# Performance work log

Hardware: AMD Instinct MI355X
Metric: run time of the kernel (lower is better)

Reference implementation:

```python
import jax, jax.numpy as jnp
import numpy as np

N_NODES = 20000
N_EDGES = 640000
C_IN = 128      # num_node_features
K_FOLDS = 8     # num_edge_features
FILTERS = 128


def setup_inputs() -> dict:
    key = jax.random.key(0)
    k1, k2, k3, k4, k5, k6 = jax.random.split(key, 6)
    node_features = jax.random.normal(k1, (N_NODES, C_IN), dtype=jnp.float32)
    edge_features = jax.random.uniform(k2, (K_FOLDS, N_EDGES), dtype=jnp.float32)
    rows = jax.random.randint(k3, (N_EDGES,), 0, N_NODES)
    cols = jax.random.randint(k4, (N_EDGES,), 0, N_NODES)
    indices = jnp.stack([rows, cols], axis=1).astype(jnp.int64)
    # glorot_uniform kernel [K, C_in, filters]
    limit = np.sqrt(6.0 / (C_IN + FILTERS))
    kernel = jax.random.uniform(k5, (K_FOLDS, C_IN, FILTERS), dtype=jnp.float32,
                                minval=-limit, maxval=limit)
    bias = jnp.zeros((FILTERS,), dtype=jnp.float32)
    return {
        "node_features": node_features,
        "edge_features": edge_features,
        "kernel": kernel,
        "bias": bias,
        "indices": indices,
        "out_size": N_NODES,
    }


def reference(node_features, edge_features, kernel, bias, indices, out_size):
    # fold_conv: out[i,f] = sum_{e: row(e)=i} sum_k ef[k,e] * (x[col(e)] @ kernel[k])[f]
    row = indices[:, 0]
    col = indices[:, 1]
    xg = node_features[col]  # [E, C] gathered source-node features
    E = xg.shape[0]
    msgs = jnp.zeros((E, kernel.shape[2]), dtype=node_features.dtype)
    # Loop over the small fixed number of folds (K=8); each iteration is a
    # dense [E,C]x[C,F] matmul scaled by the per-edge fold weight.
    for k in range(kernel.shape[0]):
        msgs = msgs + (xg @ kernel[k]) * edge_features[k][:, None]
    out = jax.ops.segment_sum(msgs, row, num_segments=out_size)  # [out_size, F]
    out = out + bias  # bias_add; activation is None (linear)
    return out
```

## Files before the change

kernel.cpp:

```cpp
#include <hip/hip_runtime.h>
#include <cstddef>
#include <cstdint>

static constexpr int kNodes   = 20000;
static constexpr int kEdges   = 640000;
static constexpr int kCin     = 128;
static constexpr int kFolds   = 8;
static constexpr int kFilters = 128;
static constexpr int kKdim    = kFolds * kCin;
static constexpr int kCap     = 80;

static constexpr int kNBucket = 250;
static constexpr int kRowsPB  = 80;
static constexpr int kCapB    = 3072;
static constexpr int kBin1Blk = 160;

typedef __attribute__((ext_vector_type(8))) short v8s;
typedef __attribute__((ext_vector_type(4))) float v4f;

__device__ __forceinline__ unsigned short f2bf(float f) {
    union { float f; uint32_t u; } v; v.f = f;
    const uint32_t u = v.u;
    return (unsigned short)((u + 0x7fffu + ((u >> 16) & 1u)) >> 16);
}
__device__ __forceinline__ float bf2f(unsigned short s) {
    union { uint32_t u; float f; } v; v.u = ((uint32_t)s) << 16;
    return v.f;
}

__global__ __launch_bounds__(256) void prep_k(
    const int2*  __restrict__ idx2,
    const float* __restrict__ ef,
    const float* __restrict__ x,
    const float* __restrict__ W,
    int* __restrict__ bucketCnt,
    int2* __restrict__ pairs,
    unsigned int* __restrict__ rec,
    unsigned short* __restrict__ xb,
    unsigned short* __restrict__ Wp)
{
    const int b = blockIdx.x;
    const int t = threadIdx.x;
    if (b < 2500) {
        const int e = b * 256 + t;
        const int2 rc = idx2[e];
        union { uint4 q; unsigned int w[4]; unsigned short s[8]; } o;
        #pragma unroll
        for (int k = 0; k < kFolds; ++k)
            o.s[k] = f2bf(ef[(size_t)k * kEdges + e]);
        uint4* recp = (uint4*)(rec + (size_t)e * 8);
        recp[0] = make_uint4((unsigned)rc.y, o.w[0], o.w[1], o.w[2]);
        recp[1] = make_uint4(o.w[3], 0u, 0u, 0u);
    } else if (b < 3750) {
        const int i = (b - 2500) * 2048 + t * 8;
        const float4 a = *(const float4*)(x + i);
        const float4 c = *(const float4*)(x + i + 4);
        union { uint4 q; unsigned short s[8]; } o;
        o.s[0] = f2bf(a.x); o.s[1] = f2bf(a.y); o.s[2] = f2bf(a.z); o.s[3] = f2bf(a.w);
        o.s[4] = f2bf(c.x); o.s[5] = f2bf(c.y); o.s[6] = f2bf(c.z); o.s[7] = f2bf(c.w);
        *(uint4*)(xb + i) = o.q;
    } else if (b < 3814) {
        const int t2 = (b - 3750) * 256 + t;
        const int n  = t2 & 127;
        const int k8 = t2 >> 7;
        const int c  = k8 >> 2;
        const int q  = k8 & 3;
        union { uint4 qv; unsigned short s[8]; } o;
        #pragma unroll
        for (int j = 0; j < 8; ++j)
            o.s[j] = f2bf(W[(size_t)(k8 * 8 + j) * kFilters + n]);
        *(uint4*)(Wp + (((size_t)c * kFilters + n) * 4 + q) * 8) = o.qv;
    } else {
        __shared__ int hist[kNBucket];
        __shared__ int base[kNBucket];
        const int bb = b - 3814;
        const int e0 = bb * 4096;

        if (t < kNBucket) hist[t] = 0;
        __syncthreads();

        int rowsReg[16];
        #pragma unroll
        for (int i = 0; i < 16; ++i) {
            const int e = e0 + i * 256 + t;
            int row = -1;
            if (e < kEdges) {
                row = idx2[e].x;
                atomicAdd(&hist[row / kRowsPB], 1);
            }
            rowsReg[i] = row;
        }
        __syncthreads();

        if (t < kNBucket) {
            const int h = hist[t];
            base[t] = atomicAdd(&bucketCnt[t], h);
            hist[t] = 0;
        }
        __syncthreads();

        #pragma unroll
        for (int i = 0; i < 16; ++i) {
            const int row = rowsReg[i];
            if (row >= 0) {
                const int e  = e0 + i * 256 + t;
                const int bk = row / kRowsPB;
                const int sl = base[bk] + atomicAdd(&hist[bk], 1);
                if (sl < kCapB)
                    pairs[(size_t)bk * kCapB + sl] = make_int2(row, e);
            }
        }
    }
}

__global__ __launch_bounds__(256) void bin2_k(
    const int2* __restrict__ pairs,
    const int*  __restrict__ bucketCnt,
    int* __restrict__ ebuf,
    int* __restrict__ cnt)
{
    __shared__ int c80[kRowsPB];
    const int b = blockIdx.x;
    const int t = threadIdx.x;

    if (t < kRowsPB) c80[t] = 0;
    __syncthreads();

    int n = bucketCnt[b];
    n = n < kCapB ? n : kCapB;
    const int2* seg = pairs + (size_t)b * kCapB;

    for (int s = t; s < n; s += 256) {
        const int2 p = seg[s];
        const int rl = p.x - b * kRowsPB;
        const int c  = atomicAdd(&c80[rl], 1);
        if (c < kCap) ebuf[p.x * kCap + c] = p.y;
    }
    __syncthreads();

    if (t < kRowsPB) cnt[b * kRowsPB + t] = c80[t];
}

static constexpr int kSWS2 = 1048;

__global__ __launch_bounds__(256) void pull_k(
    const unsigned short* __restrict__ xb,
    const int*  __restrict__ ebuf,
    const unsigned int* __restrict__ rec,
    const int*  __restrict__ cnt,
    const unsigned short* __restrict__ Wp,
    const float* __restrict__ bias,
    float* __restrict__ out)
{
    __shared__ int sCol[16][kCap + 4];
    __shared__ int sDeg[16];
    __shared__ __align__(16) char arena[16 * (kCap + 4) * 8 * 4];

    float (*sEf)[kCap + 4][8] = (float(*)[kCap + 4][8])arena;
    unsigned short (*sS)[kSWS2] = (unsigned short(*)[kSWS2])arena;

    const int t  = threadIdx.x;
    const int n0 = blockIdx.x * 16;

    {
        const int g16 = t >> 4;
        const int s0  = t & 15;
        const int nn  = n0 + g16;
        int dg = cnt[nn];
        dg = dg < kCap ? dg : kCap;
        for (int s = s0; s < dg; s += 16) {
            const int e = ebuf[nn * kCap + s];
            const uint4 q0    = *(const uint4*)(rec + (size_t)e * 8);
            const unsigned w3 = rec[(size_t)e * 8 + 4];
            sCol[g16][s] = (int)q0.x;
            sEf[g16][s][0] = bf2f((unsigned short)(q0.y));
            sEf[g16][s][1] = bf2f((unsigned short)(q0.y >> 16));
            sEf[g16][s][2] = bf2f((unsigned short)(q0.z));
            sEf[g16][s][3] = bf2f((unsigned short)(q0.z >> 16));
            sEf[g16][s][4] = bf2f((unsigned short)(q0.w));
            sEf[g16][s][5] = bf2f((unsigned short)(q0.w >> 16));
            sEf[g16][s][6] = bf2f((unsigned short)(w3));
            sEf[g16][s][7] = bf2f((unsigned short)(w3 >> 16));
        }
        const int dgP = (dg + 3) & ~3;
        for (int s = dg + s0; s < dgP; s += 16) {
            sCol[g16][s] = 0;
            #pragma unroll
            for (int k = 0; k < kFolds; ++k) sEf[g16][s][k] = 0.f;
        }
        if (s0 == 0) sDeg[g16] = dg;
    }
    __syncthreads();

    const int wave = t >> 6;
    const int lane = t & 63;
    const int g    = lane >> 4;
    const int c8   = (lane & 15) * 8;
    const int ln   = wave * 4 + g;
    const int degP = (sDeg[ln] + 3) & ~3;

    float acc[8][8];
    #pragma unroll
    for (int k = 0; k < 8; ++k)
        #pragma unroll
        for (int j = 0; j < 8; ++j) acc[k][j] = 0.f;

    const unsigned short* xbase = xb + c8;

    auto proc = [&](v8s xv, int i) {
        float xf[8];
        #pragma unroll
        for (int jj = 0; jj < 8; ++jj) xf[jj] = bf2f((unsigned short)xv[jj]);
        const float4 wa = *(const float4*)&sEf[ln][i][0];
        const float4 wc = *(const float4*)&sEf[ln][i][4];
        const float w[8] = {wa.x, wa.y, wa.z, wa.w, wc.x, wc.y, wc.z, wc.w};
        #pragma unroll
        for (int k = 0; k < 8; ++k)
            #pragma unroll
            for (int jj = 0; jj < 8; ++jj)
                acc[k][jj] += w[k] * xf[jj];
    };

    v8s x0 = (v8s)0, x1 = (v8s)0, x2 = (v8s)0, x3 = (v8s)0;
    if (degP > 0) {
        x0 = *(const v8s*)(xbase + (size_t)sCol[ln][0] * kCin);
        x1 = *(const v8s*)(xbase + (size_t)sCol[ln][1] * kCin);
        x2 = *(const v8s*)(xbase + (size_t)sCol[ln][2] * kCin);
        x3 = *(const v8s*)(xbase + (size_t)sCol[ln][3] * kCin);
    }

    for (int i = 0; i < degP; i += 4) {
        const int j = (i + 4 < degP) ? (i + 4) : i;
        const v8s y0 = *(const v8s*)(xbase + (size_t)sCol[ln][j]     * kCin);
        const v8s y1 = *(const v8s*)(xbase + (size_t)sCol[ln][j + 1] * kCin);
        const v8s y2 = *(const v8s*)(xbase + (size_t)sCol[ln][j + 2] * kCin);
        const v8s y3 = *(const v8s*)(xbase + (size_t)sCol[ln][j + 3] * kCin);

        proc(x0, i); proc(x1, i + 1); proc(x2, i + 2); proc(x3, i + 3);

        x0 = y0; x1 = y1; x2 = y2; x3 = y3;
    }

    __syncthreads();
    #pragma unroll
    for (int k = 0; k < 8; ++k) {
        union { uint4 q; unsigned short s[8]; } o;
        #pragma unroll
        for (int j = 0; j < 8; ++j) o.s[j] = f2bf(acc[k][j]);
        *(uint4*)&sS[ln][k * kCin + c8] = o.q;
    }
    __syncthreads();

    const int quad = lane >> 4;
    const int r16  = lane & 15;

    v4f acc2[2];
    acc2[0] = (v4f){0.f, 0.f, 0.f, 0.f};
    acc2[1] = (v4f){0.f, 0.f, 0.f, 0.f};

    const unsigned short* wb0 = Wp + (((size_t)(wave * 32 + r16)) * 4 + quad) * 8;
    const unsigned short* wb1 = wb0 + 16 * 4 * 8;

    #pragma unroll 4
    for (int c = 0; c < 32; ++c) {
        const v8s a  = *(const v8s*)&sS[r16][c * 32 + quad * 8];
        const v8s b0 = *(const v8s*)(wb0 + (size_t)c * kFilters * 32);
        const v8s b1 = *(const v8s*)(wb1 + (size_t)c * kFilters * 32);
        acc2[0] = __builtin_amdgcn_mfma_f32_16x16x32_bf16(a, b0, acc2[0], 0, 0, 0);
        acc2[1] = __builtin_amdgcn_mfma_f32_16x16x32_bf16(a, b1, acc2[1], 0, 0, 0);
    }

    #pragma unroll
    for (int i = 0; i < 2; ++i) {
        const int n  = (wave * 2 + i) * 16 + r16;
        const float bv = bias[n];
        #pragma unroll
        for (int r = 0; r < 4; ++r) {
            const int m = n0 + quad * 4 + r;
            out[(size_t)m * kFilters + n] = acc2[i][r] + bv;
        }
    }
}

extern "C" void kernel_launch(void* const* d_in, const int* in_sizes, int n_in,
                              void* d_out, int out_size, void* d_ws, size_t ws_size,
                              hipStream_t stream) {
    const float* x    = (const float*)d_in[0];
    const float* ef   = (const float*)d_in[1];
    const float* W    = (const float*)d_in[2];
    const float* bias = (const float*)d_in[3];
    const int2*  idx2 = (const int2*)d_in[4];
    float* out = (float*)d_out;

    char* ws = (char*)d_ws;
    int2*           pairs  = (int2*)(ws);
    unsigned int*   rec    = (unsigned int*)(ws + 40960000);
    int*            ebuf   = (int*)(ws + 61440000);
    unsigned short* xb     = (unsigned short*)(ws + 67840000);
    unsigned short* Wp     = (unsigned short*)(ws + 72960000);
    int*            cnt    = (int*)(ws + 73222144);
    int*            bucketCnt = (int*)(ws + 73302144);

    hipMemsetAsync(bucketCnt, 0, kNBucket * sizeof(int), stream);

    prep_k<<<3814 + kBin1Blk, 256, 0, stream>>>(idx2, ef, x, W, bucketCnt,
                                                pairs, rec, xb, Wp);
    bin2_k<<<kNBucket, 256, 0, stream>>>(pairs, bucketCnt, ebuf, cnt);
    pull_k<<<kNodes / 16, 256, 0, stream>>>(xb, ebuf, rec, cnt, Wp, bias, out);
}
```

Before: 165.2 us.

## Fuse second binning pass into pull kernel by scanning bucket pairs directly

Removes the separate bin2 kernel that scattered edges into per-row ebuf slots. Each pull block now scans its whole 80-row bucket's pair list (up to ~2560 pairs) and keeps only edges whose rows fall in its 16-node range, placing them straight into shared memory through shared atomics. This saves one kernel launch and the ebuf/cnt global write and reread. In exchange, each bucket's pair list is read five times, once by each of its blocks, and the edge order within a row becomes nondeterministic.

```diff
diff --git a/kernel.cpp b/kernel.cpp
--- a/kernel.cpp
+++ b/kernel.cpp
@@ -113,75 +113,63 @@
     }
 }
 
-__global__ __launch_bounds__(256) void bin2_k(
+static constexpr int kSWS2 = 1048;
+
+__global__ __launch_bounds__(256) void pull_k(
+    const unsigned short* __restrict__ xb,
     const int2* __restrict__ pairs,
     const int*  __restrict__ bucketCnt,
-    int* __restrict__ ebuf,
-    int* __restrict__ cnt)
-{
-    __shared__ int c80[kRowsPB];
-    const int b = blockIdx.x;
-    const int t = threadIdx.x;
-
-    if (t < kRowsPB) c80[t] = 0;
-    __syncthreads();
-
-    int n = bucketCnt[b];
-    n = n < kCapB ? n : kCapB;
-    const int2* seg = pairs + (size_t)b * kCapB;
-
-    for (int s = t; s < n; s += 256) {
-        const int2 p = seg[s];
-        const int rl = p.x - b * kRowsPB;
-        const int c  = atomicAdd(&c80[rl], 1);
-        if (c < kCap) ebuf[p.x * kCap + c] = p.y;
-    }
-    __syncthreads();
-
-    if (t < kRowsPB) cnt[b * kRowsPB + t] = c80[t];
-}
-
-static constexpr int kSWS2 = 1048;
-
-__global__ __launch_bounds__(256) void pull_k(
-    const unsigned short* __restrict__ xb,
-    const int*  __restrict__ ebuf,
     const unsigned int* __restrict__ rec,
-    const int*  __restrict__ cnt,
     const unsigned short* __restrict__ Wp,
     const float* __restrict__ bias,
     float* __restrict__ out)
 {
     __shared__ int sCol[16][kCap + 4];
     __shared__ int sDeg[16];
+    __shared__ int sCnt[16];
     __shared__ __align__(16) char arena[16 * (kCap + 4) * 8 * 4];
 
     float (*sEf)[kCap + 4][8] = (float(*)[kCap + 4][8])arena;
     unsigned short (*sS)[kSWS2] = (unsigned short(*)[kSWS2])arena;
 
     const int t  = threadIdx.x;
-    const int n0 = blockIdx.x * 16;
-
+    const int B  = blockIdx.x;
+    const int n0 = B * 16;
+    const int bucket = B / 5;
+
+    if (t < 16) sCnt[t] = 0;
+    __syncthreads();
+    {
+        int nseg = bucketCnt[bucket];
+        nseg = nseg < kCapB ? nseg : kCapB;
+        const int2* seg = pairs + (size_t)bucket * kCapB;
+        for (int s = t; s < nseg; s += 256) {
+            const int2 p = seg[s];
+            const unsigned rl = (unsigned)(p.x - n0);
+            if (rl < 16u) {
+                const int c = atomicAdd(&sCnt[rl], 1);
+                if (c < kCap) {
+                    const uint4 q0    = *(const uint4*)(rec + (size_t)p.y * 8);
+                    const unsigned w3 = rec[(size_t)p.y * 8 + 4];
+                    sCol[rl][c] = (int)q0.x;
+                    sEf[rl][c][0] = bf2f((unsigned short)(q0.y));
+                    sEf[rl][c][1] = bf2f((unsigned short)(q0.y >> 16));
+                    sEf[rl][c][2] = bf2f((unsigned short)(q0.z));
+                    sEf[rl][c][3] = bf2f((unsigned short)(q0.z >> 16));
+                    sEf[rl][c][4] = bf2f((unsigned short)(q0.w));
+                    sEf[rl][c][5] = bf2f((unsigned short)(q0.w >> 16));
+                    sEf[rl][c][6] = bf2f((unsigned short)(w3));
+                    sEf[rl][c][7] = bf2f((unsigned short)(w3 >> 16));
+                }
+            }
+        }
+    }
+    __syncthreads();
     {
         const int g16 = t >> 4;
         const int s0  = t & 15;
-        const int nn  = n0 + g16;
-        int dg = cnt[nn];
+        int dg = sCnt[g16];
         dg = dg < kCap ? dg : kCap;
-        for (int s = s0; s < dg; s += 16) {
-            const int e = ebuf[nn * kCap + s];
-            const uint4 q0    = *(const uint4*)(rec + (size_t)e * 8);
-            const unsigned w3 = rec[(size_t)e * 8 + 4];
-            sCol[g16][s] = (int)q0.x;
-            sEf[g16][s][0] = bf2f((unsigned short)(q0.y));
-            sEf[g16][s][1] = bf2f((unsigned short)(q0.y >> 16));
-            sEf[g16][s][2] = bf2f((unsigned short)(q0.z));
-            sEf[g16][s][3] = bf2f((unsigned short)(q0.z >> 16));
-            sEf[g16][s][4] = bf2f((unsigned short)(q0.w));
-            sEf[g16][s][5] = bf2f((unsigned short)(q0.w >> 16));
-            sEf[g16][s][6] = bf2f((unsigned short)(w3));
-            sEf[g16][s][7] = bf2f((unsigned short)(w3 >> 16));
-        }
         const int dgP = (dg + 3) & ~3;
         for (int s = dg + s0; s < dgP; s += 16) {
             sCol[g16][s] = 0;
@@ -295,16 +283,14 @@
     char* ws = (char*)d_ws;
     int2*           pairs  = (int2*)(ws);
     unsigned int*   rec    = (unsigned int*)(ws + 40960000);
-    int*            ebuf   = (int*)(ws + 61440000);
     unsigned short* xb     = (unsigned short*)(ws + 67840000);
     unsigned short* Wp     = (unsigned short*)(ws + 72960000);
-    int*            cnt    = (int*)(ws + 73222144);
     int*            bucketCnt = (int*)(ws + 73302144);
 
     hipMemsetAsync(bucketCnt, 0, kNBucket * sizeof(int), stream);
 
     prep_k<<<3814 + kBin1Blk, 256, 0, stream>>>(idx2, ef, x, W, bucketCnt,
                                                 pairs, rec, xb, Wp);
-    bin2_k<<<kNBucket, 256, 0, stream>>>(pairs, bucketCnt, ebuf, cnt);
-    pull_k<<<kNodes / 16, 256, 0, stream>>>(xb, ebuf, rec, cnt, Wp, bias, out);
-}
+    pull_k<<<kNodes / 16, 256, 0, stream>>>(xb, pairs, bucketCnt, rec,
+                                            Wp, bias, out);
+}
```

After: 164.4 us. About the same (-0.5%).
